# Kernel tuning notes

Hardware: AMD Instinct MI355X
Metric: run time of the kernel (lower is better)

Reference implementation:

```python
import jax, jax.numpy as jnp
import numpy as np

B, T, A, ACT, S, E = 32, 128, 16, 20, 512, 64


def setup_inputs() -> dict:
    key = jax.random.key(0)
    ks = jax.random.split(key, 9)
    scale = lambda k, shp, fan: (jax.random.normal(k, shp, jnp.float32) / np.sqrt(fan).astype(np.float32))
    return {
        "q_agents": jax.random.normal(ks[0], (B, T, A, ACT), jnp.float32),
        "actions": jax.random.randint(ks[1], (B, T, A, 1), 0, ACT),
        "state": jax.random.normal(ks[2], (B, T, S), jnp.float32),
        # hyper_w_1: Linear(S, E*A)
        "W_h1": scale(ks[3], (E * A, S), S), "b_h1": jnp.zeros((E * A,), jnp.float32),
        # hyper_b_1: Linear(S, E)
        "W_b1": scale(ks[4], (E, S), S), "b_b1": jnp.zeros((E,), jnp.float32),
        # hyper_w_final: Linear(S, E)
        "W_hf": scale(ks[5], (E, S), S), "b_hf": jnp.zeros((E,), jnp.float32),
        # V: Linear(S,E) -> ReLU -> Linear(E,1)
        "W_v1": scale(ks[6], (E, S), S), "b_v1": jnp.zeros((E,), jnp.float32),
        "W_v2": scale(ks[7], (1, E), E), "b_v2": jnp.zeros((1,), jnp.float32),
    }


def reference(q_agents, actions, state, W_h1, b_h1, W_b1, b_b1, W_hf, b_hf, W_v1, b_v1, W_v2, b_v2):
    bs, tt, A_, ACT_ = q_agents.shape
    E_ = W_b1.shape[0]
    N = bs * tt
    M = A_ * ACT_
    # q value of each agent's taken action: [bs, tt, A]
    qt = jnp.take_along_axis(q_agents, actions, axis=3)[..., 0]
    # counterfactual tensor: q_taken[b,t,i,act,j] = q_agents[b,t,i,act] if j==i else qt[b,t,j]
    eye = jnp.eye(A_, dtype=bool)  # [A, A]
    q_taken = jnp.where(eye[None, None, :, None, :], q_agents[..., None], qt[:, :, None, None, :])
    q_taken = q_taken.reshape(N, M, A_)  # [N, M, A]
    s = state.reshape(N, -1)  # [N, S]
    # hypernetwork weights (per-sample, shared across all M counterfactual rows)
    w1 = (s @ W_h1.T + b_h1).reshape(N, A_, E_)  # [N, A, E]
    b1 = s @ W_b1.T + b_b1                        # [N, E]
    hidden = jax.nn.elu(jnp.einsum('nma,nae->nme', q_taken, w1) + b1[:, None, :])  # [N, M, E]
    wf = s @ W_hf.T + b_hf                        # [N, E]
    v = jax.nn.relu(s @ W_v1.T + b_v1) @ W_v2.T + b_v2  # [N, 1]
    y = jnp.einsum('nme,ne->nm', hidden, wf) + v        # [N, M]
    return y.reshape(bs, tt, A_, ACT_)
```

## Files before the change

### kernel.cpp

```cpp
#include <hip/hip_runtime.h>
#include <math.h>
#include <stdint.h>

#define N_SAMPLES 4096
#define S_DIM 512
#define A_DIM 16
#define ACT_DIM 20
#define E_DIM 64
#define M_DIM 320
#define J_DIM 1216
#define JPAD 1280

using bf16x8  = __attribute__((ext_vector_type(8))) short;
using f32x4   = __attribute__((ext_vector_type(4))) float;
using ushort8 = __attribute__((ext_vector_type(8))) unsigned short;

__device__ __forceinline__ unsigned short f2bf(float x) {
    uint32_t u = __float_as_uint(x);
    u += 0x7fffu + ((u >> 16) & 1u);
    return (unsigned short)(u >> 16);
}
__device__ __forceinline__ float bf2f(unsigned short u) {
    return __uint_as_float(((uint32_t)u) << 16);
}

__global__ __launch_bounds__(256) void cvt_bf16(
    const float* __restrict__ S,
    const float* __restrict__ Wh1, const float* __restrict__ Wb1,
    const float* __restrict__ Whf, const float* __restrict__ Wv1,
    unsigned short* __restrict__ Abf, unsigned short* __restrict__ Bbf)
{
    const int A_QUADS = N_SAMPLES * S_DIM / 4;
    const int B_QUADS = JPAD * S_DIM / 4;
    int idx = blockIdx.x * 256 + threadIdx.x;
    if (idx < A_QUADS) {
        float4 v = reinterpret_cast<const float4*>(S)[idx];
        ushort4 o = { f2bf(v.x), f2bf(v.y), f2bf(v.z), f2bf(v.w) };
        reinterpret_cast<ushort4*>(Abf)[idx] = o;
    } else if (idx < A_QUADS + B_QUADS) {
        int q   = idx - A_QUADS;
        int row = q >> 7;
        int qc  = q & 127;
        ushort4 o = {0, 0, 0, 0};
        const float* src = nullptr;
        if (row < 1024)      src = Wh1 + (size_t)row * S_DIM;
        else if (row < 1088) src = Wb1 + (size_t)(row - 1024) * S_DIM;
        else if (row < 1152) src = Whf + (size_t)(row - 1088) * S_DIM;
        else if (row < 1216) src = Wv1 + (size_t)(row - 1152) * S_DIM;
        if (src) {
            float4 v = reinterpret_cast<const float4*>(src)[qc];
            o = ushort4{ f2bf(v.x), f2bf(v.y), f2bf(v.z), f2bf(v.w) };
        }
        reinterpret_cast<ushort4*>(Bbf)[q] = o;
    }
}

#define GL2L16(g, l) __builtin_amdgcn_global_load_lds(                        \
    (const __attribute__((address_space(1))) void*)(g),                      \
    (__attribute__((address_space(3))) void*)(l), 16, 0, 0)

__global__ __launch_bounds__(256, 2) void gemm_bf16(
    const unsigned short* __restrict__ Abf,
    const unsigned short* __restrict__ Bbf,
    const float* __restrict__ bh1, const float* __restrict__ bb1,
    const float* __restrict__ bhf, const float* __restrict__ bv1,
    unsigned short* __restrict__ w1_bf,
    float* __restrict__ b1_all, float* __restrict__ wf_all,
    float* __restrict__ hv_all)
{
    __shared__ short As[128 * 32];
    __shared__ short Bs[128 * 32];

    const int tid  = threadIdx.x;
    const int lane = tid & 63;
    const int wave = tid >> 6;
    const int n0 = blockIdx.x * 128;
    const int j0 = blockIdx.y * 128;

    const int gchunk = (lane & 3) ^ ((lane >> 3) & 3);
    const int srow   = wave * 32 + (lane >> 2);
    const unsigned short* gA0 = Abf + (size_t)(n0 + srow) * S_DIM + gchunk * 8;
    const unsigned short* gA1 = gA0 + 16 * S_DIM;
    const unsigned short* gB0 = Bbf + (size_t)(j0 + srow) * S_DIM + gchunk * 8;
    const unsigned short* gB1 = gB0 + 16 * S_DIM;
    short* lA0 = &As[(wave * 32) * 32];
    short* lA1 = &As[(wave * 32 + 16) * 32];
    short* lB0 = &Bs[(wave * 32) * 32];
    short* lB1 = &Bs[(wave * 32 + 16) * 32];

    const int wr = wave >> 1, wc = wave & 1;
    const int l16 = lane & 15, lk = lane >> 4;
    const int rchunk = lk ^ ((l16 >> 1) & 3);
    const short* pA = &As[(wr * 64 + l16) * 32 + rchunk * 8];
    const short* pB = &Bs[(wc * 64 + l16) * 32 + rchunk * 8];

    f32x4 acc[4][4] = {};

#pragma unroll 1
    for (int ks = 0; ks < S_DIM / 32; ++ks) {
        GL2L16(gA0, lA0);
        GL2L16(gA1, lA1);
        GL2L16(gB0, lB0);
        GL2L16(gB1, lB1);
        gA0 += 32; gA1 += 32; gB0 += 32; gB1 += 32;
        __syncthreads();
        bf16x8 a[4], b[4];
#pragma unroll
        for (int m = 0; m < 4; ++m)
            a[m] = *reinterpret_cast<const bf16x8*>(pA + m * 512);
#pragma unroll
        for (int n = 0; n < 4; ++n)
            b[n] = *reinterpret_cast<const bf16x8*>(pB + n * 512);
#pragma unroll
        for (int m = 0; m < 4; ++m)
#pragma unroll
            for (int n = 0; n < 4; ++n)
                acc[m][n] = __builtin_amdgcn_mfma_f32_16x16x32_bf16(
                    a[m], b[n], acc[m][n], 0, 0, 0);
        __syncthreads();
    }

    const int orow = n0 + wr * 64 + lk * 4;
    const int ocol = j0 + wc * 64 + l16;
#pragma unroll
    for (int m = 0; m < 4; ++m) {
#pragma unroll
        for (int n = 0; n < 4; ++n) {
            int j = ocol + n * 16;
#pragma unroll
            for (int r = 0; r < 4; ++r) {
                int row = orow + m * 16 + r;
                float val = acc[m][n][r];
                if (j < 1024)
                    w1_bf[(size_t)row * 1024 + j] = f2bf(val + bh1[j]);
                else if (j < 1088)
                    b1_all[(size_t)row * 64 + (j - 1024)] = val + bb1[j - 1024];
                else if (j < 1152)
                    wf_all[(size_t)row * 64 + (j - 1088)] = val + bhf[j - 1088];
                else if (j < J_DIM)
                    hv_all[(size_t)row * 64 + (j - 1152)] = val + bv1[j - 1152];
            }
        }
    }
}

__global__ __launch_bounds__(320) void mixer(
    const float* __restrict__ q_agents, const int* __restrict__ actions,
    const unsigned short* __restrict__ w1_bf, const float* __restrict__ b1_all,
    const float* __restrict__ wf_all, const float* __restrict__ hv_all,
    const float* __restrict__ Wv2, const float* __restrict__ bv2,
    float* __restrict__ out)
{
    const int n = blockIdx.x;
    const int tid = threadIdx.x;

    __shared__ float w1s[A_DIM][E_DIM + 1];
    __shared__ float b1s[E_DIM];
    __shared__ float wfs[E_DIM];
    __shared__ float bases[E_DIM];
    __shared__ float qts[A_DIM];
    __shared__ float v_sh;

    if (tid < 128) {
        ushort8 v = *reinterpret_cast<const ushort8*>(
            w1_bf + (size_t)n * 1024 + tid * 8);
        int a = tid >> 3, e0 = (tid & 7) * 8;
#pragma unroll
        for (int q = 0; q < 8; ++q) w1s[a][e0 + q] = bf2f((unsigned short)v[q]);
    }
    if (tid >= 192 && tid < 256) {
        int e = tid - 192;
        b1s[e] = b1_all[(size_t)n * 64 + e];
        wfs[e] = wf_all[(size_t)n * 64 + e];
    }
    if (tid >= 256 && tid < 256 + A_DIM) {
        int a = tid - 256;
        int act = actions[n * A_DIM + a];
        qts[a] = q_agents[((size_t)n * A_DIM + a) * ACT_DIM + act];
    }
    __syncthreads();

    if (tid >= 128 && tid < 192) {
        int e = tid - 128;
        float p = fmaxf(hv_all[(size_t)n * 64 + e], 0.f) * Wv2[e];
#pragma unroll
        for (int off = 32; off > 0; off >>= 1) p += __shfl_down(p, off, 64);
        if (e == 0) v_sh = p + bv2[0];
    }
    if (tid < 64) {
        float s = 0.f;
#pragma unroll
        for (int a = 0; a < A_DIM; ++a) s += qts[a] * w1s[a][tid];
        bases[tid] = s;
    }
    __syncthreads();

    {
        int m = tid;
        int i = m / ACT_DIM;
        int act = m - i * ACT_DIM;
        float delta = q_agents[((size_t)n * A_DIM + i) * ACT_DIM + act] - qts[i];
        float accv = 0.f;
#pragma unroll 8
        for (int e = 0; e < E_DIM; ++e) {
            float pre = bases[e] + delta * w1s[i][e] + b1s[e];
            float h = pre > 0.f ? pre : (__expf(pre) - 1.f);
            accv = fmaf(h, wfs[e], accv);
        }
        out[(size_t)n * M_DIM + m] = accv + v_sh;
    }
}

extern "C" void kernel_launch(void* const* d_in, const int* in_sizes, int n_in,
                              void* d_out, int out_size, void* d_ws, size_t ws_size,
                              hipStream_t stream)
{
    const float* q_agents = (const float*)d_in[0];
    const int*   actions  = (const int*)d_in[1];
    const float* state    = (const float*)d_in[2];
    const float* Wh1 = (const float*)d_in[3];
    const float* bh1 = (const float*)d_in[4];
    const float* Wb1 = (const float*)d_in[5];
    const float* bb1 = (const float*)d_in[6];
    const float* Whf = (const float*)d_in[7];
    const float* bhf = (const float*)d_in[8];
    const float* Wv1 = (const float*)d_in[9];
    const float* bv1 = (const float*)d_in[10];
    const float* Wv2 = (const float*)d_in[11];
    const float* bv2 = (const float*)d_in[12];
    float* out = (float*)d_out;

    char* ws = (char*)d_ws;
    unsigned short* Abf   = (unsigned short*)ws;
    unsigned short* Bbf   = (unsigned short*)(ws + 4194304);
    unsigned short* w1_bf = (unsigned short*)(ws + 5505024);
    float* b1_all = (float*)(ws + 5505024 + 8388608);
    float* wf_all = b1_all + (size_t)N_SAMPLES * 64;
    float* hv_all = wf_all + (size_t)N_SAMPLES * 64;

    const int total_quads = N_SAMPLES * S_DIM / 4 + JPAD * S_DIM / 4;
    hipLaunchKernelGGL(cvt_bf16, dim3((total_quads + 255) / 256), dim3(256), 0, stream,
                       state, Wh1, Wb1, Whf, Wv1, Abf, Bbf);

    dim3 g1(N_SAMPLES / 128, JPAD / 128);
    hipLaunchKernelGGL(gemm_bf16, g1, dim3(256), 0, stream,
                       Abf, Bbf, bh1, bb1, bhf, bv1,
                       w1_bf, b1_all, wf_all, hv_all);

    hipLaunchKernelGGL(mixer, dim3(N_SAMPLES), dim3(320), 0, stream,
                       q_agents, actions, w1_bf, b1_all, wf_all, hv_all,
                       Wv2, bv2, out);
}
```

Measured before the change: 56.72 us.

## Double-buffer LDS tiles in hypernetwork GEMM to overlap loads with MFMA

Doubles the LDS A/B tile buffers and restructures the K loop as a ping-pong pipeline. The global-to-LDS load for the next K slice is issued before the MFMAs on the current slice, and one barrier per stage replaces the original load-sync-compute-sync sequence. It also raises wave priority around the MFMA block with s_setprio. LDS use doubles to 32KB per block, which could limit occupancy at two blocks per CU.

Result: no change. 56.98 us (+0.5%).

```diff
diff --git a/kernel.cpp b/kernel.cpp
--- a/kernel.cpp
+++ b/kernel.cpp
@@ -68,8 +68,8 @@
     float* __restrict__ b1_all, float* __restrict__ wf_all,
     float* __restrict__ hv_all)
 {
-    __shared__ short As[128 * 32];
-    __shared__ short Bs[128 * 32];
+    __shared__ short As[2 * 128 * 32];
+    __shared__ short Bs[2 * 128 * 32];
 
     const int tid  = threadIdx.x;
     const int lane = tid & 63;
@@ -96,29 +96,45 @@
 
     f32x4 acc[4][4] = {};
 
+#define STAGE(bi, t) do {                                                     \
+        GL2L16(gA0 + (size_t)(t) * 32, lA0 + (bi) * 4096);                    \
+        GL2L16(gA1 + (size_t)(t) * 32, lA1 + (bi) * 4096);                    \
+        GL2L16(gB0 + (size_t)(t) * 32, lB0 + (bi) * 4096);                    \
+        GL2L16(gB1 + (size_t)(t) * 32, lB1 + (bi) * 4096);                    \
+    } while (0)
+
+#define COMPUTE(bi) do {                                                      \
+        bf16x8 a_[4], b_[4];                                                  \
+        _Pragma("unroll")                                                     \
+        for (int m = 0; m < 4; ++m)                                           \
+            a_[m] = *reinterpret_cast<const bf16x8*>(pA + (bi) * 4096 + m * 512); \
+        _Pragma("unroll")                                                     \
+        for (int n = 0; n < 4; ++n)                                           \
+            b_[n] = *reinterpret_cast<const bf16x8*>(pB + (bi) * 4096 + n * 512); \
+        __builtin_amdgcn_s_setprio(1);                                        \
+        _Pragma("unroll")                                                     \
+        for (int m = 0; m < 4; ++m)                                           \
+            _Pragma("unroll")                                                 \
+            for (int n = 0; n < 4; ++n)                                       \
+                acc[m][n] = __builtin_amdgcn_mfma_f32_16x16x32_bf16(          \
+                    a_[m], b_[n], acc[m][n], 0, 0, 0);                        \
+        __builtin_amdgcn_s_setprio(0);                                        \
+    } while (0)
+
+    STAGE(0, 0);
+    __syncthreads();
+
 #pragma unroll 1
-    for (int ks = 0; ks < S_DIM / 32; ++ks) {
-        GL2L16(gA0, lA0);
-        GL2L16(gA1, lA1);
-        GL2L16(gB0, lB0);
-        GL2L16(gB1, lB1);
-        gA0 += 32; gA1 += 32; gB0 += 32; gB1 += 32;
+    for (int ks = 0; ks < 16; ks += 2) {
+        STAGE(1, ks + 1);
+        COMPUTE(0);
         __syncthreads();
-        bf16x8 a[4], b[4];
-#pragma unroll
-        for (int m = 0; m < 4; ++m)
-            a[m] = *reinterpret_cast<const bf16x8*>(pA + m * 512);
-#pragma unroll
-        for (int n = 0; n < 4; ++n)
-            b[n] = *reinterpret_cast<const bf16x8*>(pB + n * 512);
-#pragma unroll
-        for (int m = 0; m < 4; ++m)
-#pragma unroll
-            for (int n = 0; n < 4; ++n)
-                acc[m][n] = __builtin_amdgcn_mfma_f32_16x16x32_bf16(
-                    a[m], b[n], acc[m][n], 0, 0, 0);
+        if (ks + 2 < 16) STAGE(0, ks + 2);
+        COMPUTE(1);
         __syncthreads();
     }
+#undef STAGE
+#undef COMPUTE
 
     const int orow = n0 + wr * 64 + lk * 4;
     const int ocol = j0 + wc * 64 + l16;
```
